# Kernel tuning notes

Hardware: AMD Instinct MI355X
Metric: run time of the kernel (lower is better)

Reference implementation:

```python
import jax, jax.numpy as jnp
import numpy as np

E = 8        # n_experts
H = 1024     # hidden_size == input_size
M = 2048     # intermediate_size
K = 2        # topk
SE = 1       # share_expert
BSZ, SEQ = 2, 1024
W_SCALE = 0.02


def setup_inputs() -> dict:
    key = jax.random.key(0)
    ks = jax.random.split(key, 9)
    return {
        "x": jax.random.normal(ks[0], (BSZ, SEQ, H), jnp.float32),
        "gate_w": jax.random.normal(ks[1], (E, H), jnp.float32) * W_SCALE,
        "beta": jnp.zeros((E,), jnp.float32),
        "gate_proj_w": jax.random.normal(ks[2], (E, H, M), jnp.float32) * W_SCALE,
        "up_proj_w": jax.random.normal(ks[3], (E, H, M), jnp.float32) * W_SCALE,
        "down_proj_w": jax.random.normal(ks[4], (E, M, H), jnp.float32) * W_SCALE,
        "shared_gate_w": jax.random.normal(ks[5], (SE, H, M), jnp.float32) * W_SCALE,
        "shared_up_w": jax.random.normal(ks[6], (SE, H, M), jnp.float32) * W_SCALE,
        "shared_down_w": jax.random.normal(ks[7], (SE, M, H), jnp.float32) * W_SCALE,
    }


def reference(x, gate_w, beta, gate_proj_w, up_proj_w, down_proj_w,
              shared_gate_w, shared_up_w, shared_down_w):
    B0, S0, H0 = x.shape
    xt = x.reshape(-1, H0)                       # [B, H], B = B0*S0 tokens
    B = xt.shape[0]

    # --- routing: top-k on (logits + beta), gate prob = sigmoid(selected logits) ---
    logits = xt @ gate_w.T                       # [B, E]
    _, idx = jax.lax.top_k(logits + beta, K)     # [B, K] expert indices
    probs = jax.nn.sigmoid(jnp.take_along_axis(logits, idx, axis=-1))  # [B, K]

    # combine weights c[b, e]: scatter top-k probs (equivalent to index_add combine)
    c = jnp.zeros((B, E), xt.dtype).at[jnp.arange(B)[:, None], idx].add(probs)

    # --- per-expert SwiGLU over all tokens, then weighted combine by c ---
    g = jnp.einsum('bh,ehm->bem', xt, gate_proj_w)   # [B, E, M]
    u = jnp.einsum('bh,ehm->bem', xt, up_proj_w)     # [B, E, M]
    h = jax.nn.silu(g) * u                           # [B, E, M]
    eo = jnp.einsum('bem,emh->beh', h, down_proj_w)  # [B, E, H]
    combined = jnp.einsum('beh,be->bh', eo, c)       # [B, H]

    # --- shared expert(s): applied to every token, no gating ---
    sg = jnp.einsum('bh,ehm->bem', xt, shared_gate_w)
    su = jnp.einsum('bh,ehm->bem', xt, shared_up_w)
    sh = jax.nn.silu(sg) * su
    shared_out = jnp.einsum('bem,emh->beh', sh, shared_down_w).sum(axis=1)  # [B, H]

    return (combined + shared_out).reshape(B0, S0, H0)
```

## Files before the change

kernel.cpp:

```cpp
#include <hip/hip_runtime.h>

#define NE 8
#define HD 1024
#define MD 2048
#define NT 2048
#define NSH 4096

typedef __attribute__((ext_vector_type(8))) short s16x8;
typedef __attribute__((ext_vector_type(4))) float f32x4;
typedef __attribute__((ext_vector_type(8))) unsigned short u16x8;
typedef __attribute__((ext_vector_type(4))) unsigned short u16x4;

__device__ __forceinline__ unsigned short f2bf(float f) {
    union { float f; unsigned int i; } v; v.f = f;
    unsigned int u = v.i;
    return (unsigned short)((u + 0x7FFFu + ((u >> 16) & 1u)) >> 16);
}
__device__ __forceinline__ float bf2f(unsigned short u) {
    union { unsigned int i; float f; } v; v.i = ((unsigned int)u) << 16; return v.f;
}

__device__ __forceinline__ void gld16(const unsigned short* g, short* l) {
    __builtin_amdgcn_global_load_lds(
        (const __attribute__((address_space(1))) unsigned int*)g,
        (__attribute__((address_space(3))) unsigned int*)l,
        16, 0, 0);
}

__global__ __launch_bounds__(256) void k_cvt(
    const float* __restrict__ s, unsigned short* __restrict__ d, int n)
{
    int i = (blockIdx.x * 256 + threadIdx.x) * 4;
    int stride = gridDim.x * 256 * 4;
    for (; i < n; i += stride) {
        float4 v = *(const float4*)(s + i);
        u16x4 o;
        o[0] = f2bf(v.x); o[1] = f2bf(v.y); o[2] = f2bf(v.z); o[3] = f2bf(v.w);
        *(u16x4*)(d + i) = o;
    }
}

__global__ __launch_bounds__(256) void k_cvt_t(
    const float* __restrict__ wr, const float* __restrict__ wsd,
    unsigned short* __restrict__ o, int K, int N, int rstride, int roff)
{
    int e = blockIdx.z;
    const float* src = (e < NE) ? wr + (size_t)e * K * N : wsd;
    unsigned short* dst = o + (size_t)e * N * K * rstride;
    int k0 = blockIdx.x * 32, n0 = blockIdx.y * 128;
    __shared__ float T[32 * 132];
    int tid = threadIdx.x;
    #pragma unroll
    for (int p = 0; p < 4; p++) {
        int k = (tid >> 5) + p * 8;
        int n4 = (tid & 31) * 4;
        float4 v = *(const float4*)(src + (size_t)(k0 + k) * N + n0 + n4);
        *(float4*)(&T[k * 132 + n4]) = v;
    }
    __syncthreads();
    #pragma unroll
    for (int p = 0; p < 2; p++) {
        int idx = tid + p * 256;
        int n = idx >> 2;
        int kq = (idx & 3) * 8;
        u16x8 r;
        #pragma unroll
        for (int j = 0; j < 8; j++) r[j] = f2bf(T[(kq + j) * 132 + n]);
        *(u16x8*)(dst + ((size_t)(n0 + n) * rstride + roff) * K + k0 + kq) = r;
    }
}

__global__ __launch_bounds__(256) void k_route(
    const float* __restrict__ x, const float* __restrict__ gw,
    const float* __restrict__ beta,
    int* __restrict__ cnt, int* __restrict__ list, int* __restrict__ slot,
    float* __restrict__ rprob)
{
    int wave = threadIdx.x >> 6, lane = threadIdx.x & 63;
    int t = blockIdx.x * 4 + wave;
    const float4* xp = (const float4*)(x + (size_t)t * HD) + lane * 4;
    float4 xv[4];
    #pragma unroll
    for (int j = 0; j < 4; j++) xv[j] = xp[j];

    float logit[NE];
    #pragma unroll
    for (int e = 0; e < NE; e++) {
        const float4* gp = (const float4*)(gw + e * HD) + lane * 4;
        float s = 0.f;
        #pragma unroll
        for (int j = 0; j < 4; j++) {
            float4 g = gp[j];
            s += xv[j].x * g.x + xv[j].y * g.y + xv[j].z * g.z + xv[j].w * g.w;
        }
        for (int off = 32; off > 0; off >>= 1) s += __shfl_xor(s, off);
        logit[e] = s;
    }
    if (lane == 0) {
        float v[NE];
        #pragma unroll
        for (int e = 0; e < NE; e++) v[e] = logit[e] + beta[e];
        int i1 = 0; float m1 = v[0];
        #pragma unroll
        for (int e = 1; e < NE; e++) if (v[e] > m1) { m1 = v[e]; i1 = e; }
        int i2 = -1; float m2 = -3.4e38f;
        #pragma unroll
        for (int e = 0; e < NE; e++) if (e != i1 && v[e] > m2) { m2 = v[e]; i2 = e; }
        if (i2 < 0) i2 = (i1 + 1) & 7;
        float p1 = 1.f / (1.f + __expf(-logit[i1]));
        float p2 = 1.f / (1.f + __expf(-logit[i2]));
        int pos1 = atomicAdd(cnt + i1, 1);
        list[i1 * NT + pos1] = t; slot[t * 2 + 0] = (i1 << 16) | pos1; rprob[t * 2 + 0] = p1;
        int pos2 = atomicAdd(cnt + i2, 1);
        list[i2 * NT + pos2] = t; slot[t * 2 + 1] = (i2 << 16) | pos2; rprob[t * 2 + 1] = p2;
    }
}

__global__ void k_scan(const int* __restrict__ cnt, int* __restrict__ base) {
    if (threadIdx.x == 0) {
        int run = 0;
        for (int e = 0; e < NE; e++) { base[e] = run; run += cnt[e]; }
        base[NE] = run;
    }
}

__global__ __launch_bounds__(256, 4) void k_gateup(
    const unsigned short* __restrict__ x,
    const unsigned short* __restrict__ wgu,
    const int* __restrict__ cnt, const int* __restrict__ base, const int* __restrict__ list,
    unsigned short* __restrict__ h)
{
    int e = blockIdx.z;
    int i0 = blockIdx.y * 128;
    int n0 = blockIdx.x * 128;
    int cnte = (e < NE) ? cnt[e] : NT;
    if (i0 >= cnte) return;
    int rbase = (e < NE) ? base[e] : NSH;
    const unsigned short* wb = wgu + (size_t)e * (2 * MD) * HD;

    __shared__ short As[2][128 * 32];
    __shared__ short Bs[2][128 * 32];
    __shared__ int tok[128];

    int tid = threadIdx.x;
    int lane = tid & 63, wave = tid >> 6;
    if (tid < 128) {
        int gi = i0 + tid;
        tok[tid] = (e < NE) ? ((gi < cnte) ? list[e * NT + gi] : list[e * NT]) : gi;
    }
    __syncthreads();

    int rr = wave * 32 + (lane >> 2);
    int kc = ((lane & 3) ^ ((lane >> 3) & 3)) * 8;
    size_t gaA0 = (size_t)tok[rr] * HD + kc;
    size_t gaA1 = (size_t)tok[rr + 16] * HD + kc;
    size_t gaB0 = (size_t)(n0 + rr) * HD + kc;
    size_t gaB1 = (size_t)(n0 + rr + 16) * HD + kc;
    int lo0 = (wave * 32) * 32, lo1 = (wave * 32 + 16) * 32;

    int wr = (wave >> 1) * 64, wc = (wave & 1) * 64;
    int m = lane & 15, q = lane >> 4;
    int sa = (m >> 1) & 3;

    f32x4 acc[4][4];
    #pragma unroll
    for (int a = 0; a < 4; a++)
        #pragma unroll
        for (int b = 0; b < 4; b++) acc[a][b] = (f32x4)0.f;

    gld16(x + gaA0, &As[0][lo0]);
    gld16(x + gaA1, &As[0][lo1]);
    gld16(wb + gaB0, &Bs[0][lo0]);
    gld16(wb + gaB1, &Bs[0][lo1]);

    int it = 0;
    for (int k0 = 0; k0 < HD; k0 += 32, it ^= 1) {
        __syncthreads();
        int nk = k0 + 32;
        if (nk < HD) {
            int nb = it ^ 1;
            gld16(x + gaA0 + nk, &As[nb][lo0]);
            gld16(x + gaA1 + nk, &As[nb][lo1]);
            gld16(wb + gaB0 + nk, &Bs[nb][lo0]);
            gld16(wb + gaB1 + nk, &Bs[nb][lo1]);
        }
        s16x8 af[4];
        #pragma unroll
        for (int ti = 0; ti < 4; ti++)
            af[ti] = *(const s16x8*)(&As[it][(wr + ti * 16 + m) * 32 + (q ^ sa) * 8]);
        #pragma unroll
        for (int tj = 0; tj < 4; tj++) {
            int nn = wc + tj * 16 + m;
            s16x8 bf = *(const s16x8*)(&Bs[it][nn * 32 + (q ^ sa) * 8]);
            #pragma unroll
            for (int ti = 0; ti < 4; ti++)
                acc[ti][tj] = __builtin_amdgcn_mfma_f32_16x16x32_bf16(af[ti], bf, acc[ti][tj], 0, 0, 0);
        }
    }
    #pragma unroll
    for (int ti = 0; ti < 4; ti++)
        #pragma unroll
        for (int tj = 0; tj < 4; tj++)
            #pragma unroll
            for (int r = 0; r < 4; r++) {
                float v = acc[ti][tj][r];
                float uo = __shfl_xor(v, 1);
                int gi = i0 + wr + ti * 16 + q * 4 + r;
                if (!(m & 1) && gi < cnte) {
                    float g = v;
                    float hv = (g / (1.f + __expf(-g))) * uo;
                    int colI = n0 + wc + tj * 16 + m;
                    h[(size_t)(rbase + gi) * MD + (colI >> 1)] = f2bf(hv);
                }
            }
}

__global__ __launch_bounds__(256, 4) void k_down(
    const unsigned short* __restrict__ wd_all,
    const int* __restrict__ cnt, const int* __restrict__ base,
    const unsigned short* __restrict__ h, unsigned short* __restrict__ eo)
{
    int e = blockIdx.z;
    int i0 = blockIdx.y * 128;
    int n0 = blockIdx.x * 128;
    int cnte = (e < NE) ? cnt[e] : NT;
    if (i0 >= cnte) return;
    int rbase = (e < NE) ? base[e] : NSH;
    const unsigned short* wd = wd_all + (size_t)e * MD * HD;

    __shared__ short As[2][128 * 32];
    __shared__ short Bd[2][128 * 32];

    int tid = threadIdx.x;
    int lane = tid & 63, wave = tid >> 6;
    int rr = wave * 32 + (lane >> 2);
    int kc = ((lane & 3) ^ ((lane >> 3) & 3)) * 8;
    size_t gaA0 = (size_t)(rbase + i0 + rr) * MD + kc;
    size_t gaA1 = (size_t)(rbase + i0 + rr + 16) * MD + kc;
    size_t gaB0 = (size_t)(n0 + rr) * MD + kc;
    size_t gaB1 = (size_t)(n0 + rr + 16) * MD + kc;
    int lo0 = (wave * 32) * 32, lo1 = (wave * 32 + 16) * 32;

    int wr = (wave >> 1) * 64, wc = (wave & 1) * 64;
    int m = lane & 15, q = lane >> 4;
    int sa = (m >> 1) & 3;

    f32x4 acc[4][4];
    #pragma unroll
    for (int a = 0; a < 4; a++)
        #pragma unroll
        for (int b = 0; b < 4; b++) acc[a][b] = (f32x4)0.f;

    gld16(h + gaA0, &As[0][lo0]);
    gld16(h + gaA1, &As[0][lo1]);
    gld16(wd + gaB0, &Bd[0][lo0]);
    gld16(wd + gaB1, &Bd[0][lo1]);

    int it = 0;
    for (int k0 = 0; k0 < MD; k0 += 32, it ^= 1) {
        __syncthreads();
        int nk = k0 + 32;
        if (nk < MD) {
            int nb = it ^ 1;
            gld16(h + gaA0 + nk, &As[nb][lo0]);
            gld16(h + gaA1 + nk, &As[nb][lo1]);
            gld16(wd + gaB0 + nk, &Bd[nb][lo0]);
            gld16(wd + gaB1 + nk, &Bd[nb][lo1]);
        }
        s16x8 af[4];
        #pragma unroll
        for (int ti = 0; ti < 4; ti++)
            af[ti] = *(const s16x8*)(&As[it][(wr + ti * 16 + m) * 32 + (q ^ sa) * 8]);
        #pragma unroll
        for (int tj = 0; tj < 4; tj++) {
            int nn = wc + tj * 16 + m;
            s16x8 bd = *(const s16x8*)(&Bd[it][nn * 32 + (q ^ sa) * 8]);
            #pragma unroll
            for (int ti = 0; ti < 4; ti++)
                acc[ti][tj] = __builtin_amdgcn_mfma_f32_16x16x32_bf16(af[ti], bd, acc[ti][tj], 0, 0, 0);
        }
    }
    #pragma unroll
    for (int ti = 0; ti < 4; ti++)
        #pragma unroll
        for (int tj = 0; tj < 4; tj++)
            #pragma unroll
            for (int r = 0; r < 4; r++) {
                int gi = i0 + wr + ti * 16 + q * 4 + r;
                if (gi < cnte) {
                    int col = n0 + wc + tj * 16 + m;
                    eo[(size_t)(rbase + gi) * HD + col] = f2bf(acc[ti][tj][r]);
                }
            }
}

__global__ __launch_bounds__(256) void k_combine(
    const unsigned short* __restrict__ eo, const int* __restrict__ slot,
    const float* __restrict__ rprob, const int* __restrict__ base,
    float* __restrict__ out)
{
    int t = blockIdx.x;
    int s0 = slot[t * 2], s1 = slot[t * 2 + 1];
    float p0 = rprob[t * 2], p1 = rprob[t * 2 + 1];
    int r0 = base[s0 >> 16] + (s0 & 0xFFFF);
    int r1 = base[s1 >> 16] + (s1 & 0xFFFF);
    int rs = NSH + t;
    int c = threadIdx.x * 4;
    u16x4 a = *(const u16x4*)(eo + (size_t)r0 * HD + c);
    u16x4 b = *(const u16x4*)(eo + (size_t)r1 * HD + c);
    u16x4 s = *(const u16x4*)(eo + (size_t)rs * HD + c);
    float4 res;
    res.x = p0 * bf2f(a[0]) + p1 * bf2f(b[0]) + bf2f(s[0]);
    res.y = p0 * bf2f(a[1]) + p1 * bf2f(b[1]) + bf2f(s[1]);
    res.z = p0 * bf2f(a[2]) + p1 * bf2f(b[2]) + bf2f(s[2]);
    res.w = p0 * bf2f(a[3]) + p1 * bf2f(b[3]) + bf2f(s[3]);
    *(float4*)(out + (size_t)t * HD + c) = res;
}

extern "C" void kernel_launch(void* const* d_in, const int* in_sizes, int n_in,
                              void* d_out, int out_size, void* d_ws, size_t ws_size,
                              hipStream_t stream)
{
    const float* x    = (const float*)d_in[0];
    const float* gw   = (const float*)d_in[1];
    const float* beta = (const float*)d_in[2];
    const float* wg   = (const float*)d_in[3];
    const float* wu   = (const float*)d_in[4];
    const float* wd   = (const float*)d_in[5];
    const float* swg  = (const float*)d_in[6];
    const float* swu  = (const float*)d_in[7];
    const float* swd  = (const float*)d_in[8];
    float* out = (float*)d_out;

    char* ws = (char*)d_ws;
    const size_t MB = (size_t)1 << 20;
    int*   cnt   = (int*)(ws + 0);
    int*   basep = (int*)(ws + 64);
    int*   list  = (int*)(ws + 1024);
    int*   slot  = (int*)(ws + 1024 + 65536);
    float* rprob = (float*)(ws + 1024 + 65536 + 16384);
    unsigned short* xb   = (unsigned short*)(ws + 1 * MB);
    unsigned short* wgut = (unsigned short*)(ws + 8 * MB);
    unsigned short* wdt  = (unsigned short*)(ws + 84 * MB);
    unsigned short* h    = (unsigned short*)(ws + 122 * MB);
    unsigned short* eo   = (unsigned short*)(ws + 146 * MB);

    hipMemsetAsync(ws, 0, 128, stream);

    const int NX = NT * HD;
    k_cvt<<<512, 256, 0, stream>>>(x, xb, NX);

    dim3 tgu(HD / 32, MD / 128, NE + 1);
    k_cvt_t<<<tgu, 256, 0, stream>>>(wg, swg, wgut, HD, MD, 2, 0);
    k_cvt_t<<<tgu, 256, 0, stream>>>(wu, swu, wgut, HD, MD, 2, 1);
    dim3 td(MD / 32, HD / 128, NE + 1);
    k_cvt_t<<<td, 256, 0, stream>>>(wd, swd, wdt, MD, HD, 1, 0);

    k_route<<<NT / 4, 256, 0, stream>>>(x, gw, beta, cnt, list, slot, rprob);
    k_scan<<<1, 64, 0, stream>>>(cnt, basep);

    dim3 g3(2 * MD / 128, NT / 128, NE + 1);
    k_gateup<<<g3, 256, 0, stream>>>(xb, wgut, cnt, basep, list, h);

    dim3 g4(HD / 128, NT / 128, NE + 1);
    k_down<<<g4, 256, 0, stream>>>(wdt, cnt, basep, h, eo);

    k_combine<<<NT, 256, 0, stream>>>(eo, slot, rprob, basep, out);
}
```

Baseline: 476.0 us.

## Store weights and h in MFMA-tiled blocked layout for contiguous LDS loads

Weights are converted into a blocked 16-row by 8-column tile layout, and gate/up interleaving now happens in a single fused conversion kernel. The h intermediate is written in the same tiled layout, with per-expert row bases padded to multiples of 16. Each wave's global-to-LDS load then reads contiguous 1KB chunks, and MFMA fragment reads from LDS need no XOR swizzle. The aim is to cut uncoalesced memory traffic, LDS bank conflicts and one conversion launch, at the cost of a scattered h store in the epilogue and a different workspace layout.

```diff
diff --git a/kernel.cpp b/kernel.cpp
--- a/kernel.cpp
+++ b/kernel.cpp
@@ -4,7 +4,7 @@
 #define HD 1024
 #define MD 2048
 #define NT 2048
-#define NSH 4096
+#define NSH 4224
 
 typedef __attribute__((ext_vector_type(8))) short s16x8;
 typedef __attribute__((ext_vector_type(4))) float f32x4;
@@ -26,6 +26,7 @@
         (__attribute__((address_space(3))) unsigned int*)l,
         16, 0, 0);
 }
+
 
 __global__ __launch_bounds__(256) void k_cvt(
     const float* __restrict__ s, unsigned short* __restrict__ d, int n)
@@ -40,33 +41,72 @@
     }
 }
 
-__global__ __launch_bounds__(256) void k_cvt_t(
+__global__ __launch_bounds__(256) void k_cvt_gu(
+    const float* __restrict__ wg, const float* __restrict__ wu,
+    const float* __restrict__ swg, const float* __restrict__ swu,
+    unsigned short* __restrict__ o)
+{
+    int e = blockIdx.z;
+    const float* sg = (e < NE) ? wg + (size_t)e * HD * MD : swg;
+    const float* su = (e < NE) ? wu + (size_t)e * HD * MD : swu;
+    unsigned short* dst = o + (size_t)e * (2 * MD) * HD;
+    int k0 = blockIdx.x * 64, n0s = blockIdx.y * 32;
+    __shared__ float T[64 * 67];
+    int tid = threadIdx.x;
+    #pragma unroll
+    for (int p = 0; p < 4; p++) {
+        int idx = p * 256 + tid;
+        int row = idx >> 4, f4 = idx & 15;
+        const float* s = (f4 < 8) ? sg : su;
+        int n4 = (f4 & 7) * 4;
+        float4 v = *(const float4*)(s + (size_t)(k0 + row) * MD + n0s + n4);
+        *(float4*)(&T[row * 67 + (f4 >> 3) * 32 + n4]) = v;
+    }
+    __syncthreads();
+    const int KC = HD / 8;
+    #pragma unroll
+    for (int p = 0; p < 2; p++) {
+        int cid = p * 256 + tid;
+        int g = cid >> 7, rem = cid & 127;
+        int kc = rem >> 4, ni = rem & 15;
+        int colT = (ni & 1) * 32 + ((g * 16 + ni) >> 1);
+        u16x8 r;
+        #pragma unroll
+        for (int j = 0; j < 8; j++) r[j] = f2bf(T[(kc * 8 + j) * 67 + colT]);
+        size_t oidx = ((size_t)((n0s >> 3) + g) * KC + (k0 >> 3) + kc) * 128 + ni * 8;
+        *(u16x8*)(dst + oidx) = r;
+    }
+}
+
+__global__ __launch_bounds__(256) void k_cvt_d(
     const float* __restrict__ wr, const float* __restrict__ wsd,
-    unsigned short* __restrict__ o, int K, int N, int rstride, int roff)
+    unsigned short* __restrict__ o)
 {
     int e = blockIdx.z;
-    const float* src = (e < NE) ? wr + (size_t)e * K * N : wsd;
-    unsigned short* dst = o + (size_t)e * N * K * rstride;
-    int k0 = blockIdx.x * 32, n0 = blockIdx.y * 128;
-    __shared__ float T[32 * 132];
+    const float* src = (e < NE) ? wr + (size_t)e * MD * HD : wsd;
+    unsigned short* dst = o + (size_t)e * MD * HD;
+    int k0 = blockIdx.x * 64, n0 = blockIdx.y * 64;
+    __shared__ float T[64 * 67];
     int tid = threadIdx.x;
     #pragma unroll
     for (int p = 0; p < 4; p++) {
-        int k = (tid >> 5) + p * 8;
-        int n4 = (tid & 31) * 4;
-        float4 v = *(const float4*)(src + (size_t)(k0 + k) * N + n0 + n4);
-        *(float4*)(&T[k * 132 + n4]) = v;
+        int idx = p * 256 + tid;
+        int row = idx >> 4, n4 = (idx & 15) * 4;
+        float4 v = *(const float4*)(src + (size_t)(k0 + row) * HD + n0 + n4);
+        *(float4*)(&T[row * 67 + n4]) = v;
     }
     __syncthreads();
+    const int KC = MD / 8;
     #pragma unroll
     for (int p = 0; p < 2; p++) {
-        int idx = tid + p * 256;
-        int n = idx >> 2;
-        int kq = (idx & 3) * 8;
+        int cid = p * 256 + tid;
+        int g = cid >> 7, rem = cid & 127;
+        int kc = rem >> 4, ni = rem & 15;
         u16x8 r;
         #pragma unroll
-        for (int j = 0; j < 8; j++) r[j] = f2bf(T[(kq + j) * 132 + n]);
-        *(u16x8*)(dst + ((size_t)(n0 + n) * rstride + roff) * K + k0 + kq) = r;
+        for (int j = 0; j < 8; j++) r[j] = f2bf(T[(kc * 8 + j) * 67 + g * 16 + ni]);
+        size_t oidx = ((size_t)((n0 >> 4) + g) * KC + (k0 >> 3) + kc) * 128 + ni * 8;
+        *(u16x8*)(dst + oidx) = r;
     }
 }
 
@@ -119,7 +159,7 @@
 __global__ void k_scan(const int* __restrict__ cnt, int* __restrict__ base) {
     if (threadIdx.x == 0) {
         int run = 0;
-        for (int e = 0; e < NE; e++) { base[e] = run; run += cnt[e]; }
+        for (int e = 0; e < NE; e++) { base[e] = run; run += (cnt[e] + 15) & ~15; }
         base[NE] = run;
     }
 }
@@ -139,7 +179,7 @@
     const unsigned short* wb = wgu + (size_t)e * (2 * MD) * HD;
 
     __shared__ short As[2][128 * 32];
-    __shared__ short Bs[2][128 * 32];
+    __shared__ short Bs[2][8 * 512];
     __shared__ int tok[128];
 
     int tid = threadIdx.x;
@@ -154,9 +194,11 @@
     int kc = ((lane & 3) ^ ((lane >> 3) & 3)) * 8;
     size_t gaA0 = (size_t)tok[rr] * HD + kc;
     size_t gaA1 = (size_t)tok[rr + 16] * HD + kc;
-    size_t gaB0 = (size_t)(n0 + rr) * HD + kc;
-    size_t gaB1 = (size_t)(n0 + rr + 16) * HD + kc;
-    int lo0 = (wave * 32) * 32, lo1 = (wave * 32 + 16) * 32;
+    const int KC = HD / 8;
+    size_t gaB0 = ((size_t)((n0 >> 4) + 2 * wave) * KC) * 128 + lane * 8;
+    size_t gaB1 = gaB0 + (size_t)KC * 128;
+    int loA0 = (wave * 32) * 32, loA1 = (wave * 32 + 16) * 32;
+    int loB0 = (2 * wave) * 512, loB1 = (2 * wave + 1) * 512;
 
     int wr = (wave >> 1) * 64, wc = (wave & 1) * 64;
     int m = lane & 15, q = lane >> 4;
@@ -168,10 +210,10 @@
         #pragma unroll
         for (int b = 0; b < 4; b++) acc[a][b] = (f32x4)0.f;
 
-    gld16(x + gaA0, &As[0][lo0]);
-    gld16(x + gaA1, &As[0][lo1]);
-    gld16(wb + gaB0, &Bs[0][lo0]);
-    gld16(wb + gaB1, &Bs[0][lo1]);
+    gld16(x + gaA0, &As[0][loA0]);
+    gld16(x + gaA1, &As[0][loA1]);
+    gld16(wb + gaB0, &Bs[0][loB0]);
+    gld16(wb + gaB1, &Bs[0][loB1]);
 
     int it = 0;
     for (int k0 = 0; k0 < HD; k0 += 32, it ^= 1) {
@@ -179,10 +221,10 @@
         int nk = k0 + 32;
         if (nk < HD) {
             int nb = it ^ 1;
-            gld16(x + gaA0 + nk, &As[nb][lo0]);
-            gld16(x + gaA1 + nk, &As[nb][lo1]);
-            gld16(wb + gaB0 + nk, &Bs[nb][lo0]);
-            gld16(wb + gaB1 + nk, &Bs[nb][lo1]);
+            gld16(x + gaA0 + nk, &As[nb][loA0]);
+            gld16(x + gaA1 + nk, &As[nb][loA1]);
+            gld16(wb + gaB0 + (size_t)nk * 16, &Bs[nb][loB0]);
+            gld16(wb + gaB1 + (size_t)nk * 16, &Bs[nb][loB1]);
         }
         s16x8 af[4];
         #pragma unroll
@@ -190,8 +232,7 @@
             af[ti] = *(const s16x8*)(&As[it][(wr + ti * 16 + m) * 32 + (q ^ sa) * 8]);
         #pragma unroll
         for (int tj = 0; tj < 4; tj++) {
-            int nn = wc + tj * 16 + m;
-            s16x8 bf = *(const s16x8*)(&Bs[it][nn * 32 + (q ^ sa) * 8]);
+            s16x8 bf = *(const s16x8*)(&Bs[it][((wave & 1) * 4 + tj) * 512 + q * 128 + m * 8]);
             #pragma unroll
             for (int ti = 0; ti < 4; ti++)
                 acc[ti][tj] = __builtin_amdgcn_mfma_f32_16x16x32_bf16(af[ti], bf, acc[ti][tj], 0, 0, 0);
@@ -209,8 +250,11 @@
                 if (!(m & 1) && gi < cnte) {
                     float g = v;
                     float hv = (g / (1.f + __expf(-g))) * uo;
-                    int colI = n0 + wc + tj * 16 + m;
-                    h[(size_t)(rbase + gi) * MD + (colI >> 1)] = f2bf(hv);
+                    int col = (n0 + wc + tj * 16 + m) >> 1;
+                    int rw = rbase + gi;
+                    size_t hi = ((size_t)(rw >> 4) * (MD >> 3) + (col >> 3)) * 128
+                              + (rw & 15) * 8 + (col & 7);
+                    h[hi] = f2bf(hv);
                 }
             }
 }
@@ -228,22 +272,21 @@
     int rbase = (e < NE) ? base[e] : NSH;
     const unsigned short* wd = wd_all + (size_t)e * MD * HD;
 
-    __shared__ short As[2][128 * 32];
-    __shared__ short Bd[2][128 * 32];
+    __shared__ short As[2][8 * 512];
+    __shared__ short Bd[2][8 * 512];
 
     int tid = threadIdx.x;
     int lane = tid & 63, wave = tid >> 6;
-    int rr = wave * 32 + (lane >> 2);
-    int kc = ((lane & 3) ^ ((lane >> 3) & 3)) * 8;
-    size_t gaA0 = (size_t)(rbase + i0 + rr) * MD + kc;
-    size_t gaA1 = (size_t)(rbase + i0 + rr + 16) * MD + kc;
-    size_t gaB0 = (size_t)(n0 + rr) * MD + kc;
-    size_t gaB1 = (size_t)(n0 + rr + 16) * MD + kc;
-    int lo0 = (wave * 32) * 32, lo1 = (wave * 32 + 16) * 32;
+    int r0 = rbase + i0;
+    const int KC = MD / 8;
+    size_t gaA0 = ((size_t)((r0 >> 4) + 2 * wave) * KC) * 128 + lane * 8;
+    size_t gaA1 = gaA0 + (size_t)KC * 128;
+    size_t gaB0 = ((size_t)((n0 >> 4) + 2 * wave) * KC) * 128 + lane * 8;
+    size_t gaB1 = gaB0 + (size_t)KC * 128;
+    int lo0 = (2 * wave) * 512, lo1 = (2 * wave + 1) * 512;
 
     int wr = (wave >> 1) * 64, wc = (wave & 1) * 64;
     int m = lane & 15, q = lane >> 4;
-    int sa = (m >> 1) & 3;
 
     f32x4 acc[4][4];
     #pragma unroll
@@ -262,19 +305,18 @@
         int nk = k0 + 32;
         if (nk < MD) {
             int nb = it ^ 1;
-            gld16(h + gaA0 + nk, &As[nb][lo0]);
-            gld16(h + gaA1 + nk, &As[nb][lo1]);
-            gld16(wd + gaB0 + nk, &Bd[nb][lo0]);
-            gld16(wd + gaB1 + nk, &Bd[nb][lo1]);
+            gld16(h + gaA0 + (size_t)nk * 16, &As[nb][lo0]);
+            gld16(h + gaA1 + (size_t)nk * 16, &As[nb][lo1]);
+            gld16(wd + gaB0 + (size_t)nk * 16, &Bd[nb][lo0]);
+            gld16(wd + gaB1 + (size_t)nk * 16, &Bd[nb][lo1]);
         }
         s16x8 af[4];
         #pragma unroll
         for (int ti = 0; ti < 4; ti++)
-            af[ti] = *(const s16x8*)(&As[it][(wr + ti * 16 + m) * 32 + (q ^ sa) * 8]);
+            af[ti] = *(const s16x8*)(&As[it][((wave >> 1) * 4 + ti) * 512 + q * 128 + m * 8]);
         #pragma unroll
         for (int tj = 0; tj < 4; tj++) {
-            int nn = wc + tj * 16 + m;
-            s16x8 bd = *(const s16x8*)(&Bd[it][nn * 32 + (q ^ sa) * 8]);
+            s16x8 bd = *(const s16x8*)(&Bd[it][((wave & 1) * 4 + tj) * 512 + q * 128 + m * 8]);
             #pragma unroll
             for (int ti = 0; ti < 4; ti++)
                 acc[ti][tj] = __builtin_amdgcn_mfma_f32_16x16x32_bf16(af[ti], bd, acc[ti][tj], 0, 0, 0);
@@ -340,21 +382,20 @@
     int*   slot  = (int*)(ws + 1024 + 65536);
     float* rprob = (float*)(ws + 1024 + 65536 + 16384);
     unsigned short* xb   = (unsigned short*)(ws + 1 * MB);
-    unsigned short* wgut = (unsigned short*)(ws + 8 * MB);
-    unsigned short* wdt  = (unsigned short*)(ws + 84 * MB);
-    unsigned short* h    = (unsigned short*)(ws + 122 * MB);
-    unsigned short* eo   = (unsigned short*)(ws + 146 * MB);
+    unsigned short* eo   = (unsigned short*)(ws + 6 * MB);
+    unsigned short* wgut = (unsigned short*)(ws + 20 * MB);
+    unsigned short* wdt  = (unsigned short*)(ws + 92 * MB);
+    unsigned short* h    = (unsigned short*)(ws + 128 * MB);
 
     hipMemsetAsync(ws, 0, 128, stream);
 
     const int NX = NT * HD;
     k_cvt<<<512, 256, 0, stream>>>(x, xb, NX);
 
-    dim3 tgu(HD / 32, MD / 128, NE + 1);
-    k_cvt_t<<<tgu, 256, 0, stream>>>(wg, swg, wgut, HD, MD, 2, 0);
-    k_cvt_t<<<tgu, 256, 0, stream>>>(wu, swu, wgut, HD, MD, 2, 1);
-    dim3 td(MD / 32, HD / 128, NE + 1);
-    k_cvt_t<<<td, 256, 0, stream>>>(wd, swd, wdt, MD, HD, 1, 0);
+    dim3 tgu(HD / 64, MD / 32, NE + 1);
+    k_cvt_gu<<<tgu, 256, 0, stream>>>(wg, wu, swg, swu, wgut);
+    dim3 td(MD / 64, HD / 64, NE + 1);
+    k_cvt_d<<<td, 256, 0, stream>>>(wd, swd, wdt);
 
     k_route<<<NT / 4, 256, 0, stream>>>(x, gw, beta, cnt, list, slot, rprob);
     k_scan<<<1, 64, 0, stream>>>(cnt, basep);
```

New measurement: 450.9 us. 1.06x faster.
